# Kernel optimization log

Hardware: AMD Instinct MI355X
Metric: run time of the kernel (lower is better)

The kernel has to match this reference:

```python
import jax, jax.numpy as jnp
import numpy as np

B, S, D_DIM = 32, 512, 1024

def setup_inputs() -> dict:
    key = jax.random.key(0)
    k1, k2, k3, k4 = jax.random.split(key, 4)
    return {
        "D": jax.random.normal(k1, (B, S, D_DIM), dtype=jnp.float32),
        "H": jax.random.normal(k2, (B, S, D_DIM), dtype=jnp.float32),
        # learned params: U is (d+1, d) (xavier-style scale), W is (2d+1,)
        # (original inits W to zeros; we use small random values so the linear
        #  term is exercised — same math either way)
        "U": jax.random.normal(k3, (D_DIM + 1, D_DIM), dtype=jnp.float32) * 0.02,
        "W": jax.random.normal(k4, (2 * D_DIM + 1,), dtype=jnp.float32) * 0.02,
    }

def reference(D, H, U, W):
    # D, H: [B, S, d]; U: [d+1, d]; W: [2d+1]
    d = H.shape[-1]
    ones = jnp.ones(D.shape[:2] + (1,), dtype=D.dtype)
    Daug = jnp.concatenate([D, ones], axis=-1)              # [B, S, d+1]
    # bilinear term: v.U.u  -> [B, Sx, Sy]
    bil = jnp.einsum('bxi,ij,byj->bxy', Daug, U, H)
    # linear term W . concat(D_aug, H): algebraically split — avoids the
    # O(B*S*S*2d) concatenated intermediate of the original implementation
    lin = (Daug @ W[:d + 1])[:, :, None] + (H @ W[d + 1:])[:, None, :]
    return bil + lin
```

## Files before the change

kernel.cpp:

```cpp
#include <hip/hip_runtime.h>


#define D_DIM 1024
#define ROWS 16384

typedef float floatx4 __attribute__((ext_vector_type(4)));
typedef __bf16 bf16x8 __attribute__((ext_vector_type(8)));

__device__ inline unsigned short f2bf(float f) {
  unsigned int u = __builtin_bit_cast(unsigned int, f);
  u = (u + 0x7FFFu + ((u >> 16) & 1u)) >> 16;
  return (unsigned short)u;
}

__device__ inline void async_load16(const void* g, void* l) {
  __builtin_amdgcn_global_load_lds(
      (const __attribute__((address_space(1))) void*)g,
      (__attribute__((address_space(3))) void*)l, 16, 0, 0);
}

__global__ __launch_bounds__(256) void cast_rows_kernel(
    const float* __restrict__ D, const float* __restrict__ H,
    const float* __restrict__ W,
    unsigned short* __restrict__ Dbf, unsigned short* __restrict__ Hbf,
    float* __restrict__ linD, float* __restrict__ linH) {
  int rowid = blockIdx.x;
  bool isH = rowid >= ROWS;
  int r = isH ? rowid - ROWS : rowid;
  const float* src = (isH ? H : D) + (size_t)r * D_DIM;
  unsigned short* dst = (isH ? Hbf : Dbf) + (size_t)r * D_DIM;
  const float* w = W + (isH ? (D_DIM + 1) : 0);
  int t = threadIdx.x;
  float4 v = ((const float4*)src)[t];
  float s = v.x * w[4*t] + v.y * w[4*t+1] + v.z * w[4*t+2] + v.w * w[4*t+3];
  ushort4 o;
  o.x = f2bf(v.x); o.y = f2bf(v.y); o.z = f2bf(v.z); o.w = f2bf(v.w);
  ((ushort4*)dst)[t] = o;
  #pragma unroll
  for (int off = 32; off > 0; off >>= 1) s += __shfl_down(s, off, 64);
  __shared__ float red[4];
  int wave = t >> 6;
  if ((t & 63) == 0) red[wave] = s;
  __syncthreads();
  if (t == 0) {
    float tot = red[0] + red[1] + red[2] + red[3];
    if (!isH) tot += W[D_DIM];
    (isH ? linH : linD)[r] = tot;
  }
}

__global__ __launch_bounds__(256) void transU_kernel(
    const float* __restrict__ U, unsigned short* __restrict__ Ut) {
  __shared__ float tile[32][33];
  int n0 = blockIdx.x * 32;
  int k0 = blockIdx.y * 32;
  int t = threadIdx.x;
  int tr = t >> 5, tc = t & 31;
  #pragma unroll
  for (int i = 0; i < 32; i += 8)
    tile[tr + i][tc] = U[(size_t)(k0 + tr + i) * D_DIM + n0 + tc];
  __syncthreads();
  #pragma unroll
  for (int i = 0; i < 32; i += 8)
    Ut[(size_t)(n0 + tr + i) * D_DIM + k0 + tc] = f2bf(tile[tc][tr + i]);
}

__device__ inline void gemm_core_swz(
    const unsigned short* __restrict__ A, const unsigned short* __restrict__ Bt,
    int m0, int n0, unsigned short* As, unsigned short* Bs,
    floatx4 (&acc)[4][4]) {
  const int K = D_DIM;
  int tid = threadIdx.x;
  int l = tid & 63, wave = tid >> 6;
  int quad = l >> 4, lrow = l & 15;
  int wm = wave >> 1, wn = wave & 1;

  int srow = 8 * wave + (l >> 3);
  int sq = (l & 7) ^ (l >> 3);
  const unsigned short* gA = A + (size_t)(m0 + srow) * K + sq * 8;
  const unsigned short* gB = Bt + (size_t)(n0 + srow) * K + sq * 8;

  int rl = lrow & 7, gofs = lrow >> 3;
  int baseA = wm * 512 + gofs * 64 + rl * 8;
  int baseB = wn * 512 + gofs * 64 + rl * 8;

  for (int k0 = 0; k0 < K; k0 += 64) {
    __syncthreads();
    #pragma unroll
    for (int j = 0; j < 4; ++j) {
      async_load16(gA + (size_t)(32 * j) * K + k0, As + (j * 256 + tid) * 8);
      async_load16(gB + (size_t)(32 * j) * K + k0, Bs + (j * 256 + tid) * 8);
    }
    __syncthreads();
    #pragma unroll
    for (int s = 0; s < 2; ++s) {
      int xq = (s * 4 + quad) ^ rl;
      bf16x8 a[4], b[4];
      #pragma unroll
      for (int mt = 0; mt < 4; ++mt)
        a[mt] = *(const bf16x8*)(As + (baseA + mt * 128 + xq) * 8);
      #pragma unroll
      for (int nt = 0; nt < 4; ++nt)
        b[nt] = *(const bf16x8*)(Bs + (baseB + nt * 128 + xq) * 8);
      #pragma unroll
      for (int mt = 0; mt < 4; ++mt)
        #pragma unroll
        for (int nt = 0; nt < 4; ++nt)
          acc[mt][nt] = __builtin_amdgcn_mfma_f32_16x16x32_bf16(
              a[mt], b[nt], acc[mt][nt], 0, 0, 0);
    }
  }
}

__global__ __launch_bounds__(256) void gemm1_kernel(
    const unsigned short* __restrict__ A,
    const unsigned short* __restrict__ Bt,
    const float* __restrict__ Ubias,
    unsigned short* __restrict__ T) {
  __shared__ __align__(16) unsigned short As[128 * 64];
  __shared__ __align__(16) unsigned short Bs[128 * 64];
  int m0 = blockIdx.x * 128, n0 = blockIdx.y * 128;
  int tid = threadIdx.x;
  int lane = tid & 63, wave = tid >> 6;
  int quad = lane >> 4, lrow = lane & 15;
  int wm = wave >> 1, wn = wave & 1;

  floatx4 acc[4][4] = {};
  gemm_core_swz(A, Bt, m0, n0, As, Bs, acc);

  #pragma unroll
  for (int mt = 0; mt < 4; ++mt)
    #pragma unroll
    for (int nt = 0; nt < 4; ++nt) {
      int row = m0 + wm * 64 + mt * 16 + quad * 4;
      int col = n0 + wn * 64 + nt * 16 + lrow;
      float bias = Ubias[col];
      #pragma unroll
      for (int rr = 0; rr < 4; ++rr)
        T[(size_t)(row + rr) * D_DIM + col] = f2bf(acc[mt][nt][rr] + bias);
    }
}

__global__ __launch_bounds__(256) void gemm2_kernel(
    const unsigned short* __restrict__ Tg,
    const unsigned short* __restrict__ Hbf,
    const float* __restrict__ linD, const float* __restrict__ linH,
    float* __restrict__ out) {
  __shared__ __align__(16) unsigned short As[128 * 64];
  __shared__ __align__(16) unsigned short Bs[128 * 64];
  int b = blockIdx.x;
  int t = blockIdx.y;
  int m0 = (t >> 2) * 128, n0 = (t & 3) * 128;
  const unsigned short* A = Tg + (size_t)b * 512 * D_DIM;
  const unsigned short* Bt = Hbf + (size_t)b * 512 * D_DIM;
  int tid = threadIdx.x;
  int lane = tid & 63, wave = tid >> 6;
  int quad = lane >> 4, lrow = lane & 15;
  int wm = wave >> 1, wn = wave & 1;

  floatx4 acc[4][4] = {};
  gemm_core_swz(A, Bt, m0, n0, As, Bs, acc);

  #pragma unroll
  for (int mt = 0; mt < 4; ++mt)
    #pragma unroll
    for (int nt = 0; nt < 4; ++nt) {
      int row = m0 + wm * 64 + mt * 16 + quad * 4;
      int col = n0 + wn * 64 + nt * 16 + lrow;
      float lh = linH[b * 512 + col];
      #pragma unroll
      for (int rr = 0; rr < 4; ++rr) {
        float v = acc[mt][nt][rr] + linD[b * 512 + row + rr] + lh;
        out[((size_t)b * 512 + row + rr) * 512 + col] = v;
      }
    }
}

extern "C" void kernel_launch(void* const* d_in, const int* in_sizes, int n_in,
                              void* d_out, int out_size, void* d_ws, size_t ws_size,
                              hipStream_t stream) {
  const float* D = (const float*)d_in[0];
  const float* H = (const float*)d_in[1];
  const float* U = (const float*)d_in[2];
  const float* W = (const float*)d_in[3];
  float* out = (float*)d_out;

  char* ws = (char*)d_ws;
  unsigned short* Dbf = (unsigned short*)ws; ws += (size_t)ROWS * D_DIM * 2;
  unsigned short* Hbf = (unsigned short*)ws; ws += (size_t)ROWS * D_DIM * 2;
  unsigned short* Tbf = (unsigned short*)ws; ws += (size_t)ROWS * D_DIM * 2;
  unsigned short* Ut  = (unsigned short*)ws; ws += (size_t)D_DIM * D_DIM * 2;
  float* linD = (float*)ws;                  ws += (size_t)ROWS * 4;
  float* linH = (float*)ws;                  ws += (size_t)ROWS * 4;

  cast_rows_kernel<<<dim3(2 * ROWS), 256, 0, stream>>>(D, H, W, Dbf, Hbf, linD, linH);
  transU_kernel<<<dim3(32, 32), 256, 0, stream>>>(U, Ut);
  gemm1_kernel<<<dim3(128, 8), 256, 0, stream>>>(Dbf, Ut, U + (size_t)D_DIM * D_DIM, Tbf);
  gemm2_kernel<<<dim3(32, 16), 256, 0, stream>>>(Tbf, Hbf, linD, linH, out);
}
```

Measured before the change: 223.0 us.

## Fold H linear term into GEMM bias and merge prep kernels

After: 229.4 us. 1.03x slower.

```diff
diff --git a/kernel.cpp b/kernel.cpp
--- a/kernel.cpp
+++ b/kernel.cpp
@@ -19,50 +19,54 @@
       (__attribute__((address_space(3))) void*)l, 16, 0, 0);
 }
 
-__global__ __launch_bounds__(256) void cast_rows_kernel(
+__global__ __launch_bounds__(256) void prep_kernel(
     const float* __restrict__ D, const float* __restrict__ H,
-    const float* __restrict__ W,
+    const float* __restrict__ U, const float* __restrict__ W,
     unsigned short* __restrict__ Dbf, unsigned short* __restrict__ Hbf,
-    float* __restrict__ linD, float* __restrict__ linH) {
-  int rowid = blockIdx.x;
-  bool isH = rowid >= ROWS;
-  int r = isH ? rowid - ROWS : rowid;
-  const float* src = (isH ? H : D) + (size_t)r * D_DIM;
-  unsigned short* dst = (isH ? Hbf : Dbf) + (size_t)r * D_DIM;
-  const float* w = W + (isH ? (D_DIM + 1) : 0);
-  int t = threadIdx.x;
-  float4 v = ((const float4*)src)[t];
-  float s = v.x * w[4*t] + v.y * w[4*t+1] + v.z * w[4*t+2] + v.w * w[4*t+3];
-  ushort4 o;
-  o.x = f2bf(v.x); o.y = f2bf(v.y); o.z = f2bf(v.z); o.w = f2bf(v.w);
-  ((ushort4*)dst)[t] = o;
-  #pragma unroll
-  for (int off = 32; off > 0; off >>= 1) s += __shfl_down(s, off, 64);
-  __shared__ float red[4];
-  int wave = t >> 6;
-  if ((t & 63) == 0) red[wave] = s;
-  __syncthreads();
-  if (t == 0) {
-    float tot = red[0] + red[1] + red[2] + red[3];
-    if (!isH) tot += W[D_DIM];
-    (isH ? linH : linD)[r] = tot;
+    unsigned short* __restrict__ Ut, float* __restrict__ Ubias,
+    float* __restrict__ linD) {
+  __shared__ float tile[32][33];
+  int bid = blockIdx.x;
+  int tid = threadIdx.x;
+  if (bid < 8192) {
+    bool isH = bid >= 4096;
+    int wave = tid >> 6, lane = tid & 63;
+    int r = ((isH ? bid - 4096 : bid) << 2) + wave;
+    const float* src = (isH ? H : D) + (size_t)r * D_DIM;
+    unsigned short* dst = (isH ? Hbf : Dbf) + (size_t)r * D_DIM;
+    float s = 0.f;
+    #pragma unroll
+    for (int i = 0; i < 4; ++i) {
+      int c = lane + 64 * i;
+      float4 v = ((const float4*)src)[c];
+      ushort4 o;
+      o.x = f2bf(v.x); o.y = f2bf(v.y); o.z = f2bf(v.z); o.w = f2bf(v.w);
+      ((ushort4*)dst)[c] = o;
+      if (!isH) {
+        float4 wv = ((const float4*)W)[c];
+        s += v.x * wv.x + v.y * wv.y + v.z * wv.z + v.w * wv.w;
+      }
+    }
+    if (!isH) {
+      #pragma unroll
+      for (int off = 32; off > 0; off >>= 1) s += __shfl_down(s, off, 64);
+      if (lane == 0) linD[r] = s + W[D_DIM];
+    }
+  } else if (bid < 9216) {
+    int t = bid - 8192;
+    int n0 = (t & 31) * 32, k0 = (t >> 5) * 32;
+    int tr = tid >> 5, tc = tid & 31;
+    #pragma unroll
+    for (int i = 0; i < 32; i += 8)
+      tile[tr + i][tc] = U[(size_t)(k0 + tr + i) * D_DIM + n0 + tc];
+    __syncthreads();
+    #pragma unroll
+    for (int i = 0; i < 32; i += 8)
+      Ut[(size_t)(n0 + tr + i) * D_DIM + k0 + tc] = f2bf(tile[tc][tr + i]);
+  } else {
+    int j = (bid - 9216) * 256 + tid;
+    Ubias[j] = U[(size_t)D_DIM * D_DIM + j] + W[D_DIM + 1 + j];
   }
-}
-
-__global__ __launch_bounds__(256) void transU_kernel(
-    const float* __restrict__ U, unsigned short* __restrict__ Ut) {
-  __shared__ float tile[32][33];
-  int n0 = blockIdx.x * 32;
-  int k0 = blockIdx.y * 32;
-  int t = threadIdx.x;
-  int tr = t >> 5, tc = t & 31;
-  #pragma unroll
-  for (int i = 0; i < 32; i += 8)
-    tile[tr + i][tc] = U[(size_t)(k0 + tr + i) * D_DIM + n0 + tc];
-  __syncthreads();
-  #pragma unroll
-  for (int i = 0; i < 32; i += 8)
-    Ut[(size_t)(n0 + tr + i) * D_DIM + k0 + tc] = f2bf(tile[tc][tr + i]);
 }
 
 __device__ inline void gemm_core_swz(
@@ -144,7 +148,7 @@
 __global__ __launch_bounds__(256) void gemm2_kernel(
     const unsigned short* __restrict__ Tg,
     const unsigned short* __restrict__ Hbf,
-    const float* __restrict__ linD, const float* __restrict__ linH,
+    const float* __restrict__ linD,
     float* __restrict__ out) {
   __shared__ __align__(16) unsigned short As[128 * 64];
   __shared__ __align__(16) unsigned short Bs[128 * 64];
@@ -167,10 +171,9 @@
     for (int nt = 0; nt < 4; ++nt) {
       int row = m0 + wm * 64 + mt * 16 + quad * 4;
       int col = n0 + wn * 64 + nt * 16 + lrow;
-      float lh = linH[b * 512 + col];
       #pragma unroll
       for (int rr = 0; rr < 4; ++rr) {
-        float v = acc[mt][nt][rr] + linD[b * 512 + row + rr] + lh;
+        float v = acc[mt][nt][rr] + linD[b * 512 + row + rr];
         out[((size_t)b * 512 + row + rr) * 512 + col] = v;
       }
     }
@@ -190,11 +193,10 @@
   unsigned short* Hbf = (unsigned short*)ws; ws += (size_t)ROWS * D_DIM * 2;
   unsigned short* Tbf = (unsigned short*)ws; ws += (size_t)ROWS * D_DIM * 2;
   unsigned short* Ut  = (unsigned short*)ws; ws += (size_t)D_DIM * D_DIM * 2;
+  float* Ubias = (float*)ws;                 ws += (size_t)D_DIM * 4;
   float* linD = (float*)ws;                  ws += (size_t)ROWS * 4;
-  float* linH = (float*)ws;                  ws += (size_t)ROWS * 4;
-
-  cast_rows_kernel<<<dim3(2 * ROWS), 256, 0, stream>>>(D, H, W, Dbf, Hbf, linD, linH);
-  transU_kernel<<<dim3(32, 32), 256, 0, stream>>>(U, Ut);
-  gemm1_kernel<<<dim3(128, 8), 256, 0, stream>>>(Dbf, Ut, U + (size_t)D_DIM * D_DIM, Tbf);
-  gemm2_kernel<<<dim3(32, 16), 256, 0, stream>>>(Tbf, Hbf, linD, linH, out);
-}
+
+  prep_kernel<<<dim3(9220), 256, 0, stream>>>(D, H, U, W, Dbf, Hbf, Ut, Ubias, linD);
+  gemm1_kernel<<<dim3(128, 8), 256, 0, stream>>>(Dbf, Ut, Ubias, Tbf);
+  gemm2_kernel<<<dim3(32, 16), 256, 0, stream>>>(Tbf, Hbf, linD, out);
+}
```
